# Optimization experiments

Hardware: AMD Instinct MI355X
Metric: run time of the kernel (lower is better)

## Reference

```python
import jax, jax.numpy as jnp
import numpy as np

B, S, D, N, C = 32, 1024, 256, 32, 64
ROUTING_ITERS = 3


def setup_inputs() -> dict:
    key = jax.random.key(0)
    k1, k2 = jax.random.split(key)
    x = jax.random.normal(k1, (B, S, D), dtype=jnp.float32)
    W = jax.random.normal(k2, (N, D, C), dtype=jnp.float32) * 0.1
    return {"x": x, "W": W}


def _squash(s, eps=1e-8):
    # s: [B, N, C]; squash along last dim
    sq_norm = jnp.sum(s * s, axis=-1, keepdims=True)
    return (sq_norm / (1.0 + sq_norm)) * s / jnp.sqrt(sq_norm + eps)


def reference(x, W):
    # Prediction vectors: u_hat[b,s,n,c] = sum_d x[b,s,d] * W[n,d,c]
    u_hat = jnp.einsum('bsd,ndc->bsnc', x, W)  # [B, S, N, C]
    b_logits = jnp.zeros(u_hat.shape[:3], dtype=u_hat.dtype)  # [B, S, N]
    v = None
    for i in range(ROUTING_ITERS):
        c = jax.nn.softmax(b_logits, axis=2)               # [B, S, N]
        s = jnp.einsum('bsn,bsnc->bnc', c, u_hat)          # [B, N, C]
        v = _squash(s)                                      # [B, N, C]
        if i < ROUTING_ITERS - 1:
            agreement = jnp.einsum('bsnc,bnc->bsn', u_hat, v)
            b_logits = b_logits + agreement
    return v
```

## Files before the change

kernel.cpp:

```cpp
#include <hip/hip_runtime.h>
#include <math.h>

namespace {
constexpr int B_ = 32, S_ = 1024, D_ = 256, N_ = 32, C_ = 64;
constexpr int NC_ = N_ * C_;
constexpr int XP_ = 16;

typedef __bf16 bf16x8 __attribute__((ext_vector_type(8)));
typedef __bf16 bf16x4 __attribute__((ext_vector_type(4)));
typedef float floatx4 __attribute__((ext_vector_type(4)));

constexpr int XS_ = 264;
constexpr int CS_ = 72;
}

extern "C" __global__ __launch_bounds__(256) void k_stage(
    const float* __restrict__ x, float* __restrict__ xsum_part) {
  const int b = blockIdx.x, sb = blockIdx.y, t = threadIdx.x;
  const float* xb = x + ((size_t)b * S_ + sb * 64) * D_;
  float a = 0.f;
  #pragma unroll 8
  for (int s = 0; s < 64; ++s) a += xb[s * D_ + t];
  xsum_part[((size_t)b * XP_ + sb) * D_ + t] = a;
}

extern "C" __global__ __launch_bounds__(256) void k_small(
    const float* __restrict__ z, const float* __restrict__ W,
    float* __restrict__ t_fp, __bf16* __restrict__ t_bhi,
    __bf16* __restrict__ t_blo, float* __restrict__ vout,
    float* __restrict__ yzero,
    int P, int zb, int zp, int zn, float scale, int accum, int final_) {
  __shared__ float zloc[256];
  __shared__ float sq_red[4][64];
  __shared__ float v_lds[64];
  const int b = blockIdx.x, n = blockIdx.y, t = threadIdx.x;

  float a = 0.f;
  for (int p = 0; p < P; ++p) a += z[(size_t)b * zb + (size_t)p * zp + n * zn + t];
  zloc[t] = a;
  if (yzero) yzero[((size_t)b * N_ + n) * D_ + t] = 0.f;
  __syncthreads();

  const int c = t & 63, dq = t >> 6;
  const float* Wn = W + (size_t)n * (D_ * C_);
  float s = 0.f;
  #pragma unroll 8
  for (int dd = 0; dd < 64; ++dd) {
    int d = dq * 64 + dd;
    s += zloc[d] * Wn[d * 64 + c];
  }
  sq_red[dq][c] = s;
  __syncthreads();

  if (t < 64) {
    float sc = (sq_red[0][t] + sq_red[1][t] + sq_red[2][t] + sq_red[3][t]) * scale;
    float sq = sc * sc;
    #pragma unroll
    for (int m = 1; m <= 32; m <<= 1) sq += __shfl_xor(sq, m);
    float scl = sq / ((1.f + sq) * sqrtf(sq + 1e-8f));
    float v = sc * scl;
    v_lds[t] = v;
    if (final_) vout[(size_t)b * NC_ + n * 64 + t] = v;
  }
  __syncthreads();

  if (!final_) {
    const float4* W4 = (const float4*)Wn + t * 16;
    float acc = 0.f;
    #pragma unroll
    for (int q = 0; q < 16; ++q) {
      float4 wv = W4[q];
      acc += wv.x * v_lds[q * 4] + wv.y * v_lds[q * 4 + 1] +
             wv.z * v_lds[q * 4 + 2] + wv.w * v_lds[q * 4 + 3];
    }
    size_t idx = ((size_t)b * N_ + n) * D_ + t;
    float tf = acc + (accum ? t_fp[idx] : 0.f);
    t_fp[idx] = tf;
    __bf16 hi = (__bf16)tf;
    t_bhi[idx] = hi;
    t_blo[idx] = (__bf16)(tf - (float)hi);
  }
}

extern "C" __global__ __launch_bounds__(256) void k_pass(
    const float* __restrict__ x, const __bf16* __restrict__ t_bhi,
    const __bf16* __restrict__ t_blo, float* __restrict__ y) {
  __shared__ __align__(16) __bf16 x_lds[64 * XS_];
  __shared__ __align__(16) __bf16 c_Th[N_ * CS_];
  __shared__ __align__(16) __bf16 c_Tl[N_ * CS_];
  const int b = blockIdx.x, ch = blockIdx.y;
  const int t = threadIdx.x, w = t >> 6, lane = t & 63;
  const int quad = lane >> 4, l16 = lane & 15;

  const float* xb = x + ((size_t)b * S_ + ch * 64) * D_;
  #pragma unroll
  for (int i = 0; i < 16; ++i) {
    int pos = i * 1024 + t * 4;
    int row = pos >> 8, col = pos & 255;
    float4 f = *(const float4*)(xb + row * D_ + col);
    bf16x4 p4;
    p4[0] = (__bf16)f.x; p4[1] = (__bf16)f.y;
    p4[2] = (__bf16)f.z; p4[3] = (__bf16)f.w;
    *(bf16x4*)(x_lds + row * XS_ + col) = p4;
  }
  __syncthreads();

  const __bf16* tb_h = t_bhi + (size_t)b * 8192;
  const __bf16* tb_l = t_blo + (size_t)b * 8192;
  floatx4 acc[2];
  acc[0] = (floatx4){0.f, 0.f, 0.f, 0.f};
  acc[1] = (floatx4){0.f, 0.f, 0.f, 0.f};
  const int sbase = w * 16;
  #pragma unroll
  for (int k0 = 0; k0 < 256; k0 += 32) {
    int ks = k0 + quad * 8;
    bf16x8 bfrag = *(const bf16x8*)(x_lds + (sbase + l16) * XS_ + ks);
    #pragma unroll
    for (int i = 0; i < 2; ++i) {
      bf16x8 ah = *(const bf16x8*)(tb_h + (i * 16 + l16) * 256 + ks);
      bf16x8 al = *(const bf16x8*)(tb_l + (i * 16 + l16) * 256 + ks);
      acc[i] = __builtin_amdgcn_mfma_f32_16x16x32_bf16(ah, bfrag, acc[i], 0, 0, 0);
      acc[i] = __builtin_amdgcn_mfma_f32_16x16x32_bf16(al, bfrag, acc[i], 0, 0, 0);
    }
  }
  float mx = -1e30f;
  #pragma unroll
  for (int i = 0; i < 2; ++i)
    #pragma unroll
    for (int r = 0; r < 4; ++r) mx = fmaxf(mx, acc[i][r]);
  mx = fmaxf(mx, __shfl_xor(mx, 16));
  mx = fmaxf(mx, __shfl_xor(mx, 32));
  float e_[2][4];
  float ss = 0.f;
  #pragma unroll
  for (int i = 0; i < 2; ++i)
    #pragma unroll
    for (int r = 0; r < 4; ++r) { e_[i][r] = __expf(acc[i][r] - mx); ss += e_[i][r]; }
  ss += __shfl_xor(ss, 16);
  ss += __shfl_xor(ss, 32);
  float inv = 1.f / ss;
  #pragma unroll
  for (int i = 0; i < 2; ++i)
    #pragma unroll
    for (int r = 0; r < 4; ++r) {
      float cv = e_[i][r] * inv;
      __bf16 chi = (__bf16)cv;
      int o = (i * 16 + quad * 4 + r) * CS_ + sbase + l16;
      c_Th[o] = chi;
      c_Tl[o] = (__bf16)(cv - (float)chi);
    }
  __syncthreads();

  floatx4 acc2[2][4];
  #pragma unroll
  for (int i = 0; i < 2; ++i)
    #pragma unroll
    for (int dt = 0; dt < 4; ++dt) acc2[i][dt] = (floatx4){0.f, 0.f, 0.f, 0.f};
  const int dbase = w * 64;
  #pragma unroll
  for (int k0 = 0; k0 < 64; k0 += 32) {
    int ks = k0 + quad * 8;
    bf16x8 ah[2], al[2];
    #pragma unroll
    for (int i = 0; i < 2; ++i) {
      ah[i] = *(const bf16x8*)(c_Th + (i * 16 + l16) * CS_ + ks);
      al[i] = *(const bf16x8*)(c_Tl + (i * 16 + l16) * CS_ + ks);
    }
    #pragma unroll
    for (int dt = 0; dt < 4; ++dt) {
      bf16x8 bfr;
      #pragma unroll
      for (int j8 = 0; j8 < 8; ++j8)
        bfr[j8] = x_lds[(ks + j8) * XS_ + dbase + dt * 16 + l16];
      #pragma unroll
      for (int i = 0; i < 2; ++i) {
        acc2[i][dt] = __builtin_amdgcn_mfma_f32_16x16x32_bf16(ah[i], bfr, acc2[i][dt], 0, 0, 0);
        acc2[i][dt] = __builtin_amdgcn_mfma_f32_16x16x32_bf16(al[i], bfr, acc2[i][dt], 0, 0, 0);
      }
    }
  }
  #pragma unroll
  for (int i = 0; i < 2; ++i)
    #pragma unroll
    for (int dt = 0; dt < 4; ++dt)
      #pragma unroll
      for (int r = 0; r < 4; ++r) {
        int n = i * 16 + quad * 4 + r;
        int d = dbase + dt * 16 + l16;
        atomicAdd(&y[((size_t)b * N_ + n) * D_ + d], acc2[i][dt][r]);
      }
}

extern "C" void kernel_launch(void* const* d_in, const int* in_sizes, int n_in,
                              void* d_out, int out_size, void* d_ws, size_t ws_size,
                              hipStream_t stream) {
  const float* x = (const float*)d_in[0];
  const float* W = (const float*)d_in[1];
  float* out = (float*)d_out;

  char* ws = (char*)d_ws;
  float* xsum_part = (float*)ws;
  float* y1 = (float*)(ws + 524288);
  float* y2 = y1 + B_ * N_ * D_;
  float* t_fp = y2 + B_ * N_ * D_;
  __bf16* t_bhi = (__bf16*)(t_fp + B_ * N_ * D_);
  __bf16* t_blo = t_bhi + B_ * N_ * D_;

  k_stage<<<dim3(B_, XP_), 256, 0, stream>>>(x, xsum_part);

  k_small<<<dim3(B_, N_), 256, 0, stream>>>(
      xsum_part, W, t_fp, t_bhi, t_blo, nullptr, y1,
      XP_, XP_ * D_, D_, 0, 1.f / 32.f, 0, 0);

  k_pass<<<dim3(B_, XP_), 256, 0, stream>>>(x, t_bhi, t_blo, y1);

  k_small<<<dim3(B_, N_), 256, 0, stream>>>(
      y1, W, t_fp, t_bhi, t_blo, nullptr, y2,
      1, N_ * D_, 0, D_, 1.f, 1, 0);

  k_pass<<<dim3(B_, XP_), 256, 0, stream>>>(x, t_bhi, t_blo, y2);

  k_small<<<dim3(B_, N_), 256, 0, stream>>>(
      y2, W, t_fp, t_bhi, t_blo, out, nullptr,
      1, N_ * D_, 0, D_, 1.f, 0, 1);
}
```

Measured before the change: 173.0 us.

## Fuse all routing stages into one persistent kernel with per-batch atomic barriers

Merges the staging, small, and pass kernels into a single kernel of 512 blocks, one per batch and sequence chunk. Blocks of the same batch synchronize through per-batch atomic counters that act as grid barriers. The x tile is converted to bf16 in LDS once and reused for both routing passes, and the x column sums are computed during that same load. This removes six launch boundaries and the repeated reads of x, but it relies on all 512 blocks being co-resident, otherwise the spin barriers deadlock, and it adds a memset launch.

```diff
diff --git a/kernel.cpp b/kernel.cpp
--- a/kernel.cpp
+++ b/kernel.cpp
@@ -14,33 +14,25 @@
 constexpr int CS_ = 72;
 }
 
-extern "C" __global__ __launch_bounds__(256) void k_stage(
-    const float* __restrict__ x, float* __restrict__ xsum_part) {
-  const int b = blockIdx.x, sb = blockIdx.y, t = threadIdx.x;
-  const float* xb = x + ((size_t)b * S_ + sb * 64) * D_;
-  float a = 0.f;
-  #pragma unroll 8
-  for (int s = 0; s < 64; ++s) a += xb[s * D_ + t];
-  xsum_part[((size_t)b * XP_ + sb) * D_ + t] = a;
-}
-
-extern "C" __global__ __launch_bounds__(256) void k_small(
-    const float* __restrict__ z, const float* __restrict__ W,
-    float* __restrict__ t_fp, __bf16* __restrict__ t_bhi,
-    __bf16* __restrict__ t_blo, float* __restrict__ vout,
-    float* __restrict__ yzero,
-    int P, int zb, int zp, int zn, float scale, int accum, int final_) {
-  __shared__ float zloc[256];
-  __shared__ float sq_red[4][64];
-  __shared__ float v_lds[64];
-  const int b = blockIdx.x, n = blockIdx.y, t = threadIdx.x;
-
-  float a = 0.f;
-  for (int p = 0; p < P; ++p) a += z[(size_t)b * zb + (size_t)p * zp + n * zn + t];
-  zloc[t] = a;
-  if (yzero) yzero[((size_t)b * N_ + n) * D_ + t] = 0.f;
-  __syncthreads();
-
+__device__ __forceinline__ void arrive(int* p) {
+  __syncthreads();
+  if (threadIdx.x == 0)
+    __hip_atomic_fetch_add(p, 1, __ATOMIC_ACQ_REL, __HIP_MEMORY_SCOPE_AGENT);
+}
+__device__ __forceinline__ void wait16(int* p) {
+  if (threadIdx.x == 0) {
+    while (__hip_atomic_load(p, __ATOMIC_ACQUIRE, __HIP_MEMORY_SCOPE_AGENT) < 16)
+      __builtin_amdgcn_s_sleep(2);
+  }
+  __syncthreads();
+}
+
+__device__ __forceinline__ void small_one(
+    int b, int n, const float* __restrict__ W, float scale, int accum,
+    int final_, float* __restrict__ t_fp, __bf16* __restrict__ t_bhi,
+    __bf16* __restrict__ t_blo, float* __restrict__ out,
+    const float* zloc, float* sq_red, float* v_lds) {
+  const int t = threadIdx.x;
   const int c = t & 63, dq = t >> 6;
   const float* Wn = W + (size_t)n * (D_ * C_);
   float s = 0.f;
@@ -49,21 +41,19 @@
     int d = dq * 64 + dd;
     s += zloc[d] * Wn[d * 64 + c];
   }
-  sq_red[dq][c] = s;
-  __syncthreads();
-
+  sq_red[dq * 64 + c] = s;
+  __syncthreads();
   if (t < 64) {
-    float sc = (sq_red[0][t] + sq_red[1][t] + sq_red[2][t] + sq_red[3][t]) * scale;
+    float sc = (sq_red[t] + sq_red[64 + t] + sq_red[128 + t] + sq_red[192 + t]) * scale;
     float sq = sc * sc;
     #pragma unroll
     for (int m = 1; m <= 32; m <<= 1) sq += __shfl_xor(sq, m);
     float scl = sq / ((1.f + sq) * sqrtf(sq + 1e-8f));
     float v = sc * scl;
     v_lds[t] = v;
-    if (final_) vout[(size_t)b * NC_ + n * 64 + t] = v;
-  }
-  __syncthreads();
-
+    if (final_) out[(size_t)b * NC_ + n * 64 + t] = v;
+  }
+  __syncthreads();
   if (!final_) {
     const float4* W4 = (const float4*)Wn + t * 16;
     float acc = 0.f;
@@ -80,33 +70,17 @@
     t_bhi[idx] = hi;
     t_blo[idx] = (__bf16)(tf - (float)hi);
   }
-}
-
-extern "C" __global__ __launch_bounds__(256) void k_pass(
-    const float* __restrict__ x, const __bf16* __restrict__ t_bhi,
-    const __bf16* __restrict__ t_blo, float* __restrict__ y) {
-  __shared__ __align__(16) __bf16 x_lds[64 * XS_];
-  __shared__ __align__(16) __bf16 c_Th[N_ * CS_];
-  __shared__ __align__(16) __bf16 c_Tl[N_ * CS_];
-  const int b = blockIdx.x, ch = blockIdx.y;
+  __syncthreads();
+}
+
+__device__ __forceinline__ void pass_phase(
+    int b, const __bf16* __restrict__ t_bhi, const __bf16* __restrict__ t_blo,
+    float* __restrict__ y, const __bf16* x_lds, __bf16* c_Th, __bf16* c_Tl) {
   const int t = threadIdx.x, w = t >> 6, lane = t & 63;
   const int quad = lane >> 4, l16 = lane & 15;
-
-  const float* xb = x + ((size_t)b * S_ + ch * 64) * D_;
-  #pragma unroll
-  for (int i = 0; i < 16; ++i) {
-    int pos = i * 1024 + t * 4;
-    int row = pos >> 8, col = pos & 255;
-    float4 f = *(const float4*)(xb + row * D_ + col);
-    bf16x4 p4;
-    p4[0] = (__bf16)f.x; p4[1] = (__bf16)f.y;
-    p4[2] = (__bf16)f.z; p4[3] = (__bf16)f.w;
-    *(bf16x4*)(x_lds + row * XS_ + col) = p4;
-  }
-  __syncthreads();
-
   const __bf16* tb_h = t_bhi + (size_t)b * 8192;
   const __bf16* tb_l = t_blo + (size_t)b * 8192;
+
   floatx4 acc[2];
   acc[0] = (floatx4){0.f, 0.f, 0.f, 0.f};
   acc[1] = (floatx4){0.f, 0.f, 0.f, 0.f};
@@ -189,6 +163,103 @@
         int d = dbase + dt * 16 + l16;
         atomicAdd(&y[((size_t)b * N_ + n) * D_ + d], acc2[i][dt][r]);
       }
+  __syncthreads();
+}
+
+extern "C" __global__ __launch_bounds__(256) void k_fused(
+    const float* __restrict__ x, const float* __restrict__ W,
+    float* __restrict__ xsum_part, float* __restrict__ y1,
+    float* __restrict__ y2, float* __restrict__ t_fp,
+    __bf16* __restrict__ t_bhi, __bf16* __restrict__ t_blo,
+    int* __restrict__ cnt, float* __restrict__ out) {
+  __shared__ __align__(16) __bf16 x_lds[64 * XS_];
+  __shared__ __align__(16) __bf16 c_Th[N_ * CS_];
+  __shared__ __align__(16) __bf16 c_Tl[N_ * CS_];
+  float* zloc = (float*)c_Th;
+  float* sq_red = (float*)c_Th + 256;
+  float* v_lds = (float*)c_Th + 512;
+  float* ph0red = (float*)c_Tl;
+
+  const int bidx = blockIdx.x;
+  const int b = bidx >> 4, ch = bidx & 15;
+  const int t = threadIdx.x;
+  int* c0 = cnt + b;
+  int* ct1 = cnt + 32 + b;
+  int* cy1 = cnt + 64 + b;
+  int* ct2 = cnt + 96 + b;
+  int* cy2 = cnt + 128 + b;
+
+  {
+    const float* xb = x + ((size_t)b * S_ + ch * 64) * D_;
+    float xp[4] = {0.f, 0.f, 0.f, 0.f};
+    #pragma unroll
+    for (int i = 0; i < 16; ++i) {
+      int pos = i * 1024 + t * 4;
+      int row = pos >> 8, col = (t & 63) * 4;
+      float4 f = *(const float4*)(xb + pos);
+      bf16x4 p4;
+      p4[0] = (__bf16)f.x; p4[1] = (__bf16)f.y;
+      p4[2] = (__bf16)f.z; p4[3] = (__bf16)f.w;
+      *(bf16x4*)(x_lds + row * XS_ + col) = p4;
+      xp[0] += f.x; xp[1] += f.y; xp[2] += f.z; xp[3] += f.w;
+    }
+    const int w = t >> 6, col = (t & 63) * 4;
+    #pragma unroll
+    for (int k = 0; k < 4; ++k) ph0red[w * 256 + col + k] = xp[k];
+    __syncthreads();
+    xsum_part[((size_t)b * XP_ + ch) * D_ + t] =
+        ph0red[t] + ph0red[256 + t] + ph0red[512 + t] + ph0red[768 + t];
+    #pragma unroll
+    for (int k = 0; k < 2; ++k) {
+      y1[(size_t)b * (N_ * D_) + ch * 512 + k * 256 + t] = 0.f;
+      y2[(size_t)b * (N_ * D_) + ch * 512 + k * 256 + t] = 0.f;
+    }
+  }
+  arrive(c0);
+  wait16(c0);
+
+  {
+    float a = 0.f;
+    #pragma unroll
+    for (int p = 0; p < XP_; ++p) a += xsum_part[((size_t)b * XP_ + p) * D_ + t];
+    __syncthreads();
+    zloc[t] = a;
+    __syncthreads();
+    small_one(b, ch * 2, W, 1.f / 32.f, 0, 0, t_fp, t_bhi, t_blo, nullptr,
+              zloc, sq_red, v_lds);
+    small_one(b, ch * 2 + 1, W, 1.f / 32.f, 0, 0, t_fp, t_bhi, t_blo, nullptr,
+              zloc, sq_red, v_lds);
+  }
+  arrive(ct1);
+  wait16(ct1);
+
+  pass_phase(b, t_bhi, t_blo, y1, x_lds, c_Th, c_Tl);
+  arrive(cy1);
+  wait16(cy1);
+
+  #pragma unroll
+  for (int u = 0; u < 2; ++u) {
+    int n = ch * 2 + u;
+    zloc[t] = y1[((size_t)b * N_ + n) * D_ + t];
+    __syncthreads();
+    small_one(b, n, W, 1.f, 1, 0, t_fp, t_bhi, t_blo, nullptr,
+              zloc, sq_red, v_lds);
+  }
+  arrive(ct2);
+  wait16(ct2);
+
+  pass_phase(b, t_bhi, t_blo, y2, x_lds, c_Th, c_Tl);
+  arrive(cy2);
+  wait16(cy2);
+
+  #pragma unroll
+  for (int u = 0; u < 2; ++u) {
+    int n = ch * 2 + u;
+    zloc[t] = y2[((size_t)b * N_ + n) * D_ + t];
+    __syncthreads();
+    small_one(b, n, W, 1.f, 0, 1, t_fp, t_bhi, t_blo, out,
+              zloc, sq_red, v_lds);
+  }
 }
 
 extern "C" void kernel_launch(void* const* d_in, const int* in_sizes, int n_in,
@@ -205,22 +276,9 @@
   float* t_fp = y2 + B_ * N_ * D_;
   __bf16* t_bhi = (__bf16*)(t_fp + B_ * N_ * D_);
   __bf16* t_blo = t_bhi + B_ * N_ * D_;
-
-  k_stage<<<dim3(B_, XP_), 256, 0, stream>>>(x, xsum_part);
-
-  k_small<<<dim3(B_, N_), 256, 0, stream>>>(
-      xsum_part, W, t_fp, t_bhi, t_blo, nullptr, y1,
-      XP_, XP_ * D_, D_, 0, 1.f / 32.f, 0, 0);
-
-  k_pass<<<dim3(B_, XP_), 256, 0, stream>>>(x, t_bhi, t_blo, y1);
-
-  k_small<<<dim3(B_, N_), 256, 0, stream>>>(
-      y1, W, t_fp, t_bhi, t_blo, nullptr, y2,
-      1, N_ * D_, 0, D_, 1.f, 1, 0);
-
-  k_pass<<<dim3(B_, XP_), 256, 0, stream>>>(x, t_bhi, t_blo, y2);
-
-  k_small<<<dim3(B_, N_), 256, 0, stream>>>(
-      y2, W, t_fp, t_bhi, t_blo, out, nullptr,
-      1, N_ * D_, 0, D_, 1.f, 0, 1);
-}
+  int* cnt = (int*)(t_blo + B_ * N_ * D_);
+
+  hipMemsetAsync(cnt, 0, 5 * 32 * sizeof(int), stream);
+  k_fused<<<dim3(B_ * XP_), dim3(256), 0, stream>>>(
+      x, W, xsum_part, y1, y2, t_fp, t_bhi, t_blo, cnt, out);
+}
```

Measured after the change: 311.4 us. +80.0%, slower.
